# Optimization experiments

Measured on AMD Instinct MI355X. Metric: run time of the kernel, lower is better.

Reference implementation:

```python
import jax, jax.numpy as jnp
import numpy as np

SQRT2 = 1.4142135623730951
INV_SQRT_2PI = 0.3989422804014327

def Phi(x):
    # standard normal CDF
    return 0.5 * (1.0 + jax.lax.erf(x / SQRT2))

def phi(x):
    # standard normal pdf
    return INV_SQRT_2PI * jnp.exp(-0.5 * x * x)

def phip(x):
    # derivative of the standard normal pdf
    return -x * phi(x)


def setup_inputs() -> dict:
    key = jax.random.key(0)
    k1, k2, k3 = jax.random.split(key, 3)
    bs, n, c, d = 4, 256, 96, 2
    xin = jax.random.normal(k1, (bs, n, d), dtype=jnp.float32)
    meanin = jax.random.normal(k2, (bs, n, c), dtype=jnp.float32)
    # SPD spatial covariance: A A^T / n + 0.5 I (eigenvalues >> 1e-6)
    A = jax.random.normal(k3, (bs, n, n), dtype=jnp.float32)
    kin = A @ jnp.swapaxes(A, -1, -2) / n + 0.5 * jnp.eye(n, dtype=jnp.float32)
    return {"xin": xin, "meanin": meanin, "kin": kin}


def reference(xin, meanin, kin):
    bs, n, c = meanin.shape
    eye = jnp.eye(n, dtype=kin.dtype)
    kin = kin + eye * 1e-6
    kdiag = jnp.diagonal(kin, axis1=-2, axis2=-1)            # (bs,n)
    stdin = jnp.sqrt(jnp.clip(kdiag[..., None], 1e-8))       # (bs,n,1)
    z = meanin / stdin
    Phis = Phi(z)
    phis = phi(z)
    Eh = meanin * Phis + stdin * phis                        # (bs,n,c)

    # 2x2 matrix K12 per (i,j): [[k_ii, k_ij], [k_ji, k_jj]] -- kept as scalars
    m00 = kdiag[:, :, None]                                  # (bs,n,1) -> broadcast (bs,n,n)
    m11 = kdiag[:, None, :]
    m01 = kin
    m10 = jnp.swapaxes(kin, -1, -2)

    # matrix square root of 2x2 SPD: (M + sqrt(det) I) / sqrt(tr + 2 sqrt(det))
    det = m00 * m11 - m01 * m10
    tr = m00 + m11
    s = jnp.sqrt(jnp.clip(det, 1e-8))
    t = jnp.clip(jnp.sqrt(tr + 2.0 * s), 1e-8)
    s00 = (m00 + s) / t
    s01 = m01 / t
    s10 = m10 / t
    s11 = (m11 + s) / t

    # inverse of the 2x2 sqrt
    dS = jnp.clip(s00 * s11 - s01 * s10, 1e-8)
    i00 = s11 / dS
    i01 = -s01 / dS
    i10 = -s10 / dS
    i11 = s00 / dS

    mi = meanin[:, :, None, :]                               # (bs,n,1,c)
    mj = meanin[:, None, :, :]                               # (bs,1,n,c)

    u1 = i00[..., None] * mi + i01[..., None] * mj           # (bs,n,n,c)
    u2 = i10[..., None] * mi + i11[..., None] * mj
    Phi1 = Phi(u1)
    Phi2 = Phi(u2)
    p1 = phi(u1)
    p2 = phi(u2)

    Psi = Phi1 * Phi2
    psi1 = p1 * Phi2
    psi2 = Phi1 * p2

    EhhT_Psi = (mi * mj + kin[..., None]) * Psi
    EhhT_psi1 = (mj * s00[..., None] + mi * s10[..., None]) * psi1
    EhhT_psi2 = (mj * s01[..., None] + mi * s11[..., None]) * psi2

    SHPhiS11 = s00[..., None] * s01[..., None] * phip(u1) * Phi2
    SHPhiS12 = s01[..., None] * s01[..., None] * p1 * p2
    SHPhiS22 = s01[..., None] * s11[..., None] * Phi1 * phip(u2)
    SHPhiS = SHPhiS11 + 2.0 * SHPhiS12 + SHPhiS22

    EhhT = EhhT_Psi + (EhhT_psi1 + EhhT_psi2) + SHPhiS
    covar = (EhhT - Eh[:, :, None, :] * Eh[:, None, :, :]).mean(-1)   # (bs,n,n)

    dvals = jnp.clip(
        ((meanin ** 2 + stdin ** 2) * Phis + meanin * stdin * phis - Eh ** 2).mean(-1),
        1e-6,
    )                                                        # (bs,n)
    diag_covar = dvals[..., None] * eye                      # diag_embed
    full_covar = jnp.where(diag_covar > 1e-7, diag_covar, covar)
    return (xin, Eh, full_covar + eye * 1e-6)
```

## Files before the change

kernel.cpp:

```cpp
#include <hip/hip_runtime.h>
#include <math.h>

#define BSZ 4
#define NN  256
#define CC  96
#define TT  16
#define NTILES 136
#define LSTR 52

#define XIN_OFF  0
#define EH_OFF   2048
#define COV_OFF  100352

#define INV_SQRT_2PI 0.3989422804014327f
#define EXP2C       -0.7213475204444817f
#define PHI_P   0.33267253f
#define PHI_C1  0.1740121f
#define PHI_C2 -0.0479399f
#define PHI_C3  0.3739278f

__device__ __forceinline__ float phi_from_exp_s(float u, float e) {
    float t  = __builtin_amdgcn_rcpf(__builtin_fmaf(PHI_P, fabsf(u), 1.0f));
    float hp = __builtin_fmaf(__builtin_fmaf(PHI_C3, t, PHI_C2), t, PHI_C1) * t * e;
    return 0.5f + __builtin_copysignf(0.5f - hp, u);
}

__device__ __forceinline__ int tri_offset(int k) {
    return k * TT - (k * (k - 1)) / 2;
}
__device__ __forceinline__ void tri_decode(int t, int& ti, int& tj) {
    float disc = 1089.0f - 8.0f * (float)t;
    ti = (int)((33.0f - __builtin_amdgcn_sqrtf(disc)) * 0.5f);
    while (tri_offset(ti + 1) <= t) ++ti;
    while (tri_offset(ti) > t) --ti;
    tj = ti + (t - tri_offset(ti));
}

__global__ __launch_bounds__(128) void relu_cov_row(
    const float* __restrict__ xin, const float* __restrict__ meanin,
    const float* __restrict__ kin, float* __restrict__ out)
{
    const int row = blockIdx.x;
    const int b   = row >> 8;
    const int i   = row & (NN - 1);
    const int tid = threadIdx.x;

    const float kd   = kin[((size_t)b * NN + i) * NN + i] + 1e-6f;
    const float var  = fmaxf(kd, 1e-8f);
    const float stdv = __builtin_amdgcn_sqrtf(var);
    const float rstd = __builtin_amdgcn_rcpf(stdv);

    float dterm = 0.0f;
    if (tid < CC) {
        float m  = meanin[(size_t)row * CC + tid];
        float z  = m * rstd;
        float e  = __builtin_amdgcn_exp2f(z * z * EXP2C);
        float ph = INV_SQRT_2PI * e;
        float Ph = phi_from_exp_s(z, e);
        float Eh = m * Ph + stdv * ph;
        out[EH_OFF + (size_t)row * CC + tid] = Eh;
        dterm = (m * m + var) * Ph + m * stdv * ph - Eh * Eh;
    } else if (tid < CC + 2) {
        int dd = tid - CC;
        out[XIN_OFF + (size_t)row * 2 + dd] = xin[(size_t)row * 2 + dd];
    }

    float v = dterm;
    v += __shfl_down(v, 32, 64);
    v += __shfl_down(v, 16, 64);
    v += __shfl_down(v,  8, 64);
    v += __shfl_down(v,  4, 64);
    v += __shfl_down(v,  2, 64);
    v += __shfl_down(v,  1, 64);
    __shared__ float wsum[2];
    if ((tid & 63) == 0) wsum[tid >> 6] = v;
    __syncthreads();
    if (tid == 0) {
        float dval = fmaxf((wsum[0] + wsum[1]) * (1.0f / 96.0f), 1e-6f);
        out[COV_OFF + ((size_t)b * NN + i) * NN + i] = dval + 1e-6f;
    }
}

__global__ __launch_bounds__(256) void relu_cov_pair(
    const float* __restrict__ meanin, const float* __restrict__ kin,
    const float* __restrict__ Eh, float* __restrict__ partial)
{
    const int bx = blockIdx.x;
    const int b  = bx / NTILES;
    const int t  = bx - b * NTILES;
    const int ch = blockIdx.y;
    const int p  = threadIdx.x;

    int ti, tj;
    tri_decode(t, ti, tj);

    __shared__ __align__(16) float lds[4 * TT * LSTR];
    float* const smi = lds;
    float* const sEi = lds + TT * LSTR;
    float* const smj = lds + 2 * TT * LSTR;
    float* const sEj = lds + 3 * TT * LSTR;

    {
        int k = p;
#pragma unroll
        for (int it = 0; it < 3; ++it, k += 256) {
            int arr = k / 192;
            int rem = k - arr * 192;
            int r   = rem / 12;
            int q   = rem - r * 12;
            const float* src = (arr == 0 || arr == 2) ? meanin : Eh;
            int row = ((arr < 2) ? ti : tj) * TT + r;
            float4 v = *((const float4*)(src + ((size_t)(b * NN + row)) * CC + ch * 48) + q);
            float* dst = lds + arr * (TT * LSTR) + r * LSTR + q * 4;
            *(float4*)dst = v;
        }
    }
    __syncthreads();

    const int i_loc = p >> 4;
    const int j_loc = p & 15;
    const int i = ti * TT + i_loc;
    const int j = tj * TT + j_loc;

    const float* kb  = kin + (size_t)b * NN * NN;
    const float  m00 = kb[i * (NN + 1)] + 1e-6f;
    const float  m11 = kb[j * (NN + 1)] + 1e-6f;
    const float  m01 = kb[i * NN + j];

    const float det = __builtin_fmaf(-m01, m01, m00 * m11);
    const float s   = __builtin_amdgcn_sqrtf(fmaxf(det, 1e-8f));
    const float tt  = fmaxf(__builtin_amdgcn_sqrtf(m00 + m11 + 2.0f * s), 1e-8f);
    const float rt  = __builtin_amdgcn_rcpf(tt);
    const float s00 = (m00 + s) * rt;
    const float s01 = m01 * rt;
    const float s11 = (m11 + s) * rt;
    const float dS  = fmaxf(__builtin_fmaf(-s01, s01, s00 * s11), 1e-8f);
    const float rdS = __builtin_amdgcn_rcpf(dS);
    const float i00 = s11 * rdS;
    const float i01 = -s01 * rdS;
    const float i11 = s00 * rdS;
    const float qd = -INV_SQRT_2PI * s01 * s01 * s01 * rdS;
    const float qj =  INV_SQRT_2PI * s00 * s00 * s11 * rdS;
    const float qi =  INV_SQRT_2PI * s00 * s11 * s11 * rdS;
    const float c2 = 2.0f * INV_SQRT_2PI * INV_SQRT_2PI * s01 * s01;

    const float* Lmi = smi + i_loc * LSTR;
    const float* LEi = sEi + i_loc * LSTR;
    const float* Lmj = smj + j_loc * LSTR;
    const float* LEj = sEj + j_loc * LSTR;

    float acc0 = 0.0f, acc1 = 0.0f, acc2 = 0.0f, acc3 = 0.0f;

    auto elem = [&](float mi, float mjv, float Ei, float Ej, float& acc) {
        float u1 = __builtin_fmaf(i01, mjv, i00 * mi);
        float u2 = __builtin_fmaf(i11, mjv, i01 * mi);
        float e1 = __builtin_amdgcn_exp2f(u1 * u1 * EXP2C);
        float e2 = __builtin_amdgcn_exp2f(u2 * u2 * EXP2C);
        float d1 = __builtin_fmaf(PHI_P, fabsf(u1), 1.0f);
        float d2 = __builtin_fmaf(PHI_P, fabsf(u2), 1.0f);
        float rp = __builtin_amdgcn_rcpf(d1 * d2);
        float t1 = d2 * rp;
        float t2 = d1 * rp;
        float hp1 = __builtin_fmaf(__builtin_fmaf(PHI_C3, t1, PHI_C2), t1, PHI_C1) * t1 * e1;
        float hp2 = __builtin_fmaf(__builtin_fmaf(PHI_C3, t2, PHI_C2), t2, PHI_C1) * t2 * e2;
        float Phi1 = 0.5f + __builtin_copysignf(0.5f - hp1, u1);
        float Phi2 = 0.5f + __builtin_copysignf(0.5f - hp2, u2);
        float a  = __builtin_fmaf(mi, mjv, m01);
        float bb = __builtin_fmaf(qd, mi, qj * mjv);
        float cc = __builtin_fmaf(qi, mi, qd * mjv);
        float ta = __builtin_fmaf(a,  Phi1, bb * e1);
        float tb = __builtin_fmaf(cc, Phi1, c2 * e1);
        acc = __builtin_fmaf(Phi2, ta, acc);
        acc = __builtin_fmaf(e2,   tb, acc);
        acc = __builtin_fmaf(-Ei,  Ej, acc);
    };

#pragma unroll 4
    for (int q = 0; q < 12; ++q) {
        float4 mi4 = *(const float4*)(Lmi + q * 4);
        float4 mj4 = *(const float4*)(Lmj + q * 4);
        float4 Ei4 = *(const float4*)(LEi + q * 4);
        float4 Ej4 = *(const float4*)(LEj + q * 4);
        elem(mi4.x, mj4.x, Ei4.x, Ej4.x, acc0);
        elem(mi4.y, mj4.y, Ei4.y, Ej4.y, acc1);
        elem(mi4.z, mj4.z, Ei4.z, Ej4.z, acc2);
        elem(mi4.w, mj4.w, Ei4.w, Ej4.w, acc3);
    }

    partial[((size_t)bx * 2 + ch) * 256 + p] = (acc0 + acc1) + (acc2 + acc3);
}

__global__ __launch_bounds__(256) void relu_cov_combine(
    const float* __restrict__ partial, float* __restrict__ out)
{
    const int bx = blockIdx.x;
    const int b  = bx / NTILES;
    const int t  = bx - b * NTILES;
    const int p  = threadIdx.x;

    int ti, tj;
    tri_decode(t, ti, tj);
    const int i = ti * TT + (p >> 4);
    const int j = tj * TT + (p & 15);
    if (i >= j) return;

    const float* base = partial + ((size_t)bx * 2) * 256 + p;
    float v = (base[0] + base[256]) * (1.0f / 96.0f);

    out[COV_OFF + ((size_t)(b * NN + i)) * NN + j] = v;
    out[COV_OFF + ((size_t)(b * NN + j)) * NN + i] = v;
}

extern "C" void kernel_launch(void* const* d_in, const int* in_sizes, int n_in,
                              void* d_out, int out_size, void* d_ws, size_t ws_size,
                              hipStream_t stream) {
    const float* xin    = (const float*)d_in[0];
    const float* meanin = (const float*)d_in[1];
    const float* kin    = (const float*)d_in[2];
    float* out     = (float*)d_out;
    float* partial = (float*)d_ws;

    relu_cov_row<<<BSZ * NN, 128, 0, stream>>>(xin, meanin, kin, out);
    relu_cov_pair<<<dim3(BSZ * NTILES, 2), 256, 0, stream>>>(
        meanin, kin, out + EH_OFF, partial);
    relu_cov_combine<<<BSZ * NTILES, 256, 0, stream>>>(partial, out);
}
```

Before: 77.72 us.

## Fuse row, pair and combine kernels into one tile kernel

Merges the three launches into a single kernel. Each 512-thread block loads the meanin rows for its tile pair, recomputes Eh in LDS, writes Eh, xin and the diagonal only on diagonal tiles, and splits the channel dimension across two half-blocks. The halves are reduced through shared memory, which removes the workspace partials, the separate combine pass and two launch gaps. The cost is that Eh is recomputed redundantly for every tile, and the larger LDS footprint per block may lower occupancy.

```diff
diff --git a/kernel.cpp b/kernel.cpp
--- a/kernel.cpp
+++ b/kernel.cpp
@@ -6,7 +6,8 @@
 #define CC  96
 #define TT  16
 #define NTILES 136
-#define LSTR 52
+#define RSTR 100
+#define ARR  (TT * RSTR)
 
 #define XIN_OFF  0
 #define EH_OFF   2048
@@ -36,96 +37,121 @@
     tj = ti + (t - tri_offset(ti));
 }
 
-__global__ __launch_bounds__(128) void relu_cov_row(
+__global__ __launch_bounds__(512) void relu_cov_fused(
     const float* __restrict__ xin, const float* __restrict__ meanin,
     const float* __restrict__ kin, float* __restrict__ out)
 {
-    const int row = blockIdx.x;
-    const int b   = row >> 8;
-    const int i   = row & (NN - 1);
+    const int blk = blockIdx.x;
+    const int b   = blk / NTILES;
+    const int t   = blk - b * NTILES;
     const int tid = threadIdx.x;
-
-    const float kd   = kin[((size_t)b * NN + i) * NN + i] + 1e-6f;
-    const float var  = fmaxf(kd, 1e-8f);
-    const float stdv = __builtin_amdgcn_sqrtf(var);
-    const float rstd = __builtin_amdgcn_rcpf(stdv);
-
-    float dterm = 0.0f;
-    if (tid < CC) {
-        float m  = meanin[(size_t)row * CC + tid];
-        float z  = m * rstd;
-        float e  = __builtin_amdgcn_exp2f(z * z * EXP2C);
-        float ph = INV_SQRT_2PI * e;
-        float Ph = phi_from_exp_s(z, e);
-        float Eh = m * Ph + stdv * ph;
-        out[EH_OFF + (size_t)row * CC + tid] = Eh;
-        dterm = (m * m + var) * Ph + m * stdv * ph - Eh * Eh;
-    } else if (tid < CC + 2) {
-        int dd = tid - CC;
-        out[XIN_OFF + (size_t)row * 2 + dd] = xin[(size_t)row * 2 + dd];
-    }
-
-    float v = dterm;
-    v += __shfl_down(v, 32, 64);
-    v += __shfl_down(v, 16, 64);
-    v += __shfl_down(v,  8, 64);
-    v += __shfl_down(v,  4, 64);
-    v += __shfl_down(v,  2, 64);
-    v += __shfl_down(v,  1, 64);
-    __shared__ float wsum[2];
-    if ((tid & 63) == 0) wsum[tid >> 6] = v;
-    __syncthreads();
-    if (tid == 0) {
-        float dval = fmaxf((wsum[0] + wsum[1]) * (1.0f / 96.0f), 1e-6f);
-        out[COV_OFF + ((size_t)b * NN + i) * NN + i] = dval + 1e-6f;
-    }
-}
-
-__global__ __launch_bounds__(256) void relu_cov_pair(
-    const float* __restrict__ meanin, const float* __restrict__ kin,
-    const float* __restrict__ Eh, float* __restrict__ partial)
-{
-    const int bx = blockIdx.x;
-    const int b  = bx / NTILES;
-    const int t  = bx - b * NTILES;
-    const int ch = blockIdx.y;
-    const int p  = threadIdx.x;
 
     int ti, tj;
     tri_decode(t, ti, tj);
-
-    __shared__ __align__(16) float lds[4 * TT * LSTR];
+    const bool diag = (ti == tj);
+
+    __shared__ __align__(16) float lds[4 * ARR];
+    __shared__ float red[512];
+    __shared__ float srowS[32], srowR[32], srowV[32];
     float* const smi = lds;
-    float* const sEi = lds + TT * LSTR;
-    float* const smj = lds + 2 * TT * LSTR;
-    float* const sEj = lds + 3 * TT * LSTR;
-
-    {
-        int k = p;
-#pragma unroll
-        for (int it = 0; it < 3; ++it, k += 256) {
-            int arr = k / 192;
-            int rem = k - arr * 192;
-            int r   = rem / 12;
-            int q   = rem - r * 12;
-            const float* src = (arr == 0 || arr == 2) ? meanin : Eh;
-            int row = ((arr < 2) ? ti : tj) * TT + r;
-            float4 v = *((const float4*)(src + ((size_t)(b * NN + row)) * CC + ch * 48) + q);
-            float* dst = lds + arr * (TT * LSTR) + r * LSTR + q * 4;
-            *(float4*)dst = v;
+    float* const sEi = lds + ARR;
+    float* const smj = lds + 2 * ARR;
+    float* const sEj = lds + 3 * ARR;
+
+    if (tid < 32) {
+        int row = (tid < 16) ? (ti * TT + tid) : (tj * TT + (tid - 16));
+        float kd  = kin[((size_t)(b * NN + row)) * NN + row] + 1e-6f;
+        float var = fmaxf(kd, 1e-8f);
+        float st  = __builtin_amdgcn_sqrtf(var);
+        srowV[tid] = var;
+        srowS[tid] = st;
+        srowR[tid] = __builtin_amdgcn_rcpf(st);
+    }
+#pragma unroll
+    for (int it = 0; it < 2; ++it) {
+        int k = tid + it * 512;
+        if (k < 768) {
+            int arr = k / 384;
+            int rem = k - arr * 384;
+            int r   = rem / 24;
+            int q   = rem - r * 24;
+            int row = ((arr == 0) ? ti : tj) * TT + r;
+            float4 v = *((const float4*)(meanin + ((size_t)(b * NN + row)) * CC) + q);
+            *(float4*)(lds + arr * 2 * ARR + r * RSTR + q * 4) = v;
         }
     }
     __syncthreads();
 
+#pragma unroll
+    for (int it = 0; it < 6; ++it) {
+        int k   = tid + it * 512;
+        int arr = k / 1536;
+        int rem = k - arr * 1536;
+        int r   = rem / 96;
+        int c   = rem - r * 96;
+        float m  = lds[arr * 2 * ARR + r * RSTR + c];
+        float st = srowS[arr * 16 + r];
+        float rs = srowR[arr * 16 + r];
+        float z  = m * rs;
+        float e  = __builtin_amdgcn_exp2f(z * z * EXP2C);
+        float Ph = phi_from_exp_s(z, e);
+        float Eh = __builtin_fmaf(m, Ph, st * (INV_SQRT_2PI * e));
+        lds[(arr * 2 + 1) * ARR + r * RSTR + c] = Eh;
+    }
+    __syncthreads();
+
+    if (diag) {
+#pragma unroll
+        for (int it = 0; it < 3; ++it) {
+            int k = tid + it * 512;
+            int r = k / 96, c = k - r * 96;
+            out[EH_OFF + ((size_t)(b * NN + ti * TT + r)) * CC + c] = sEi[r * RSTR + c];
+        }
+        if (tid < 32) {
+            int r = tid >> 1, d = tid & 1;
+            size_t o = ((size_t)(b * NN + ti * TT + r)) * 2 + d;
+            out[XIN_OFF + o] = xin[o];
+        }
+        {
+            int r = tid >> 5, s = tid & 31;
+            float st = srowS[r], var = srowV[r], rs = srowR[r];
+            float dsum = 0.0f;
+#pragma unroll
+            for (int dc = 0; dc < 3; ++dc) {
+                int c = s * 3 + dc;
+                float m  = smi[r * RSTR + c];
+                float Eh = sEi[r * RSTR + c];
+                float z  = m * rs;
+                float e  = __builtin_amdgcn_exp2f(z * z * EXP2C);
+                float Ph = phi_from_exp_s(z, e);
+                float ph = INV_SQRT_2PI * e;
+                float dt = __builtin_fmaf(__builtin_fmaf(m, m, var), Ph,
+                           __builtin_fmaf(m * st, ph, -Eh * Eh));
+                dsum += dt;
+            }
+            dsum += __shfl_down(dsum, 16, 32);
+            dsum += __shfl_down(dsum,  8, 32);
+            dsum += __shfl_down(dsum,  4, 32);
+            dsum += __shfl_down(dsum,  2, 32);
+            dsum += __shfl_down(dsum,  1, 32);
+            if (s == 0) {
+                float dval = fmaxf(dsum * (1.0f / 96.0f), 1e-6f);
+                int row = ti * TT + r;
+                out[COV_OFF + ((size_t)(b * NN + row)) * NN + row] = dval + 1e-6f;
+            }
+        }
+    }
+
+    const int p     = tid & 255;
+    const int h     = tid >> 8;
     const int i_loc = p >> 4;
     const int j_loc = p & 15;
     const int i = ti * TT + i_loc;
     const int j = tj * TT + j_loc;
 
-    const float* kb  = kin + (size_t)b * NN * NN;
-    const float  m00 = kb[i * (NN + 1)] + 1e-6f;
-    const float  m11 = kb[j * (NN + 1)] + 1e-6f;
-    const float  m01 = kb[i * NN + j];
+    const float m00 = srowV[i_loc];
+    const float m11 = srowV[16 + j_loc];
+    const float m01 = kin[((size_t)(b * NN + i)) * NN + j];
 
     const float det = __builtin_fmaf(-m01, m01, m00 * m11);
     const float s   = __builtin_amdgcn_sqrtf(fmaxf(det, 1e-8f));
@@ -144,10 +170,10 @@
     const float qi =  INV_SQRT_2PI * s00 * s11 * s11 * rdS;
     const float c2 = 2.0f * INV_SQRT_2PI * INV_SQRT_2PI * s01 * s01;
 
-    const float* Lmi = smi + i_loc * LSTR;
-    const float* LEi = sEi + i_loc * LSTR;
-    const float* Lmj = smj + j_loc * LSTR;
-    const float* LEj = sEj + j_loc * LSTR;
+    const float* Lmi = smi + i_loc * RSTR + h * 48;
+    const float* LEi = sEi + i_loc * RSTR + h * 48;
+    const float* Lmj = smj + j_loc * RSTR + h * 48;
+    const float* LEj = sEj + j_loc * RSTR + h * 48;
 
     float acc0 = 0.0f, acc1 = 0.0f, acc2 = 0.0f, acc3 = 0.0f;
 
@@ -187,28 +213,14 @@
         elem(mi4.w, mj4.w, Ei4.w, Ej4.w, acc3);
     }
 
-    partial[((size_t)bx * 2 + ch) * 256 + p] = (acc0 + acc1) + (acc2 + acc3);
-}
-
-__global__ __launch_bounds__(256) void relu_cov_combine(
-    const float* __restrict__ partial, float* __restrict__ out)
-{
-    const int bx = blockIdx.x;
-    const int b  = bx / NTILES;
-    const int t  = bx - b * NTILES;
-    const int p  = threadIdx.x;
-
-    int ti, tj;
-    tri_decode(t, ti, tj);
-    const int i = ti * TT + (p >> 4);
-    const int j = tj * TT + (p & 15);
-    if (i >= j) return;
-
-    const float* base = partial + ((size_t)bx * 2) * 256 + p;
-    float v = (base[0] + base[256]) * (1.0f / 96.0f);
-
-    out[COV_OFF + ((size_t)(b * NN + i)) * NN + j] = v;
-    out[COV_OFF + ((size_t)(b * NN + j)) * NN + i] = v;
+    red[tid] = (acc0 + acc1) + (acc2 + acc3);
+    __syncthreads();
+
+    if (tid < 256 && i < j) {
+        float v = (red[tid] + red[tid + 256]) * (1.0f / 96.0f);
+        out[COV_OFF + ((size_t)(b * NN + i)) * NN + j] = v;
+        out[COV_OFF + ((size_t)(b * NN + j)) * NN + i] = v;
+    }
 }
 
 extern "C" void kernel_launch(void* const* d_in, const int* in_sizes, int n_in,
@@ -217,11 +229,7 @@
     const float* xin    = (const float*)d_in[0];
     const float* meanin = (const float*)d_in[1];
     const float* kin    = (const float*)d_in[2];
-    float* out     = (float*)d_out;
-    float* partial = (float*)d_ws;
-
-    relu_cov_row<<<BSZ * NN, 128, 0, stream>>>(xin, meanin, kin, out);
-    relu_cov_pair<<<dim3(BSZ * NTILES, 2), 256, 0, stream>>>(
-        meanin, kin, out + EH_OFF, partial);
-    relu_cov_combine<<<BSZ * NTILES, 256, 0, stream>>>(partial, out);
-}
+    float* out = (float*)d_out;
+
+    relu_cov_fused<<<BSZ * NTILES, 512, 0, stream>>>(xin, meanin, kin, out);
+}
```

After: 77.19 us. About the same (-0.7%).
